# Kernel tuning notes

Measured on AMD Instinct MI355X. Metric: run time of the kernel, lower is better.

## Reference

```python
import jax, jax.numpy as jnp
import numpy as np

H = 1024   # hidden_dim
NH = 16    # num_heads
HD = H // NH  # head_dim = 64
B, S = 2, 2048
LN_EPS = 1e-5


def setup_inputs() -> dict:
    key = jax.random.key(0)
    ks = jax.random.split(key, 5)
    scale = 1.0 / np.sqrt(H)  # xavier-ish scale for stability
    return {
        "x": jax.random.normal(ks[0], (B, S, H), dtype=jnp.float32),
        "Wq": jax.random.normal(ks[1], (H, H), dtype=jnp.float32) * scale,
        "bq": jnp.zeros((H,), jnp.float32),
        "Wk": jax.random.normal(ks[2], (H, H), dtype=jnp.float32) * scale,
        "bk": jnp.zeros((H,), jnp.float32),
        "Wv": jax.random.normal(ks[3], (H, H), dtype=jnp.float32) * scale,
        "bv": jnp.zeros((H,), jnp.float32),
        "Wo": jax.random.normal(ks[4], (H, H), dtype=jnp.float32) * scale,
        "bo": jnp.zeros((H,), jnp.float32),
        "ln_gamma": jnp.ones((H,), jnp.float32),
        "ln_beta": jnp.zeros((H,), jnp.float32),
    }


def reference(x, Wq, bq, Wk, bk, Wv, bv, Wo, bo, ln_gamma, ln_beta):
    b, s, _ = x.shape
    # QKV projections, split heads: (b, nh, s, hd)
    def split_heads(t):
        return t.reshape(b, s, NH, HD).transpose(0, 2, 1, 3)
    Q = split_heads(x @ Wq + bq)
    K = split_heads(x @ Wk + bk)
    V = split_heads(x @ Wv + bv)
    # scaled dot-product with clamp (mask=None path)
    scores = jnp.einsum('bhqd,bhkd->bhqk', Q, K) / np.sqrt(HD).astype(np.float32)
    scores = jnp.clip(scores, -10000.0, 10000.0)
    attn = jax.nn.softmax(scores, axis=-1)
    # dropout is identity in eval mode
    ctx = jnp.einsum('bhqk,bhkd->bhqd', attn, V)
    ctx = ctx.transpose(0, 2, 1, 3).reshape(b, s, H)
    out = ctx @ Wo + bo
    # residual + LayerNorm
    y = out + x
    mu = jnp.mean(y, axis=-1, keepdims=True)
    var = jnp.mean(jnp.square(y - mu), axis=-1, keepdims=True)
    y = (y - mu) * jax.lax.rsqrt(var + LN_EPS)
    return y * ln_gamma + ln_beta
```

## Files before the change

kernel.cpp:

```cpp
#include <hip/hip_runtime.h>

typedef unsigned short u16;
typedef __attribute__((ext_vector_type(8))) short shortx8;
typedef __attribute__((ext_vector_type(4))) float floatx4;
typedef __attribute__((ext_vector_type(2))) unsigned uintx2;

#define GLD16(gp, lp) __builtin_amdgcn_global_load_lds( \
    (__attribute__((address_space(1))) void*)(gp), \
    (__attribute__((address_space(3))) void*)(lp), 16, 0, 0)

__device__ __forceinline__ u16 f2bf(float f) {
  union { float f; unsigned u; } v; v.f = f;
  unsigned r = v.u + 0x7FFFu + ((v.u >> 16) & 1u);
  return (u16)(r >> 16);
}

__device__ __forceinline__ unsigned bcast_u(float f) {
  union { float f; unsigned u; } v; v.f = f;
  return v.u;
}

__global__ __launch_bounds__(256) void cast_x_kernel(const float* __restrict__ x,
                                                     u16* __restrict__ xb, int n4) {
  int i = blockIdx.x * 256 + threadIdx.x;
  if (i < n4) {
    float4 v = ((const float4*)x)[i];
    ushort4 o;
    o.x = f2bf(v.x); o.y = f2bf(v.y); o.z = f2bf(v.z); o.w = f2bf(v.w);
    ((ushort4*)xb)[i] = o;
  }
}

__global__ __launch_bounds__(256) void transpose_cast_w(const float* __restrict__ Wq,
                                                        const float* __restrict__ Wk,
                                                        const float* __restrict__ Wv,
                                                        const float* __restrict__ Wo,
                                                        u16* __restrict__ Wt) {
  __shared__ u16 tile[32][33];
  int mat = blockIdx.z;
  const float* W = (mat == 0) ? Wq : (mat == 1) ? Wk : (mat == 2) ? Wv : Wo;
  u16* dst = Wt + (size_t)mat * 1024 * 1024;
  int n0 = blockIdx.x * 32, k0 = blockIdx.y * 32;
  int tx = threadIdx.x, ty = threadIdx.y;
  for (int i = 0; i < 4; ++i)
    tile[ty + i * 8][tx] = f2bf(W[(size_t)(k0 + ty + i * 8) * 1024 + n0 + tx]);
  __syncthreads();
  for (int i = 0; i < 4; ++i)
    dst[(size_t)(n0 + ty + i * 8) * 1024 + k0 + tx] = tile[tx][ty + i * 8];
}

__device__ __forceinline__ void gemm_tile_core(const u16* __restrict__ A,
                                               const u16* __restrict__ Bt,
                                               int m0, int n0,
                                               u16* As, u16* Bs,
                                               floatx4 (&acc)[4][4]) {
  const int tid = threadIdx.x;
  const int wave = tid >> 6, lane = tid & 63;
  const int lrow = lane >> 4, lcol = lane & 15;
  const int wm = wave >> 1, wn = wave & 1;

  for (int mi = 0; mi < 4; ++mi)
    for (int ni = 0; ni < 4; ++ni)
      acc[mi][ni] = (floatx4){0.f, 0.f, 0.f, 0.f};

  const u16* ap[4];
  const u16* bp[4];
  for (int l = 0; l < 4; ++l) {
    int g = (l * 4 + wave) * 64 + lane;
    int r = g >> 3, c = g & 7;
    int cc = (c ^ (r & 7)) * 8;
    ap[l] = A + (size_t)(m0 + r) * 1024 + cc;
    bp[l] = Bt + (size_t)(n0 + r) * 1024 + cc;
  }

  for (int k0 = 0; k0 < 1024; k0 += 64) {
    __syncthreads();
    for (int l = 0; l < 4; ++l) {
      GLD16(ap[l], As + (l * 4 + wave) * 512);
      GLD16(bp[l], Bs + (l * 4 + wave) * 512);
      ap[l] += 64; bp[l] += 64;
    }
    __syncthreads();
    for (int kk = 0; kk < 2; ++kk) {
      shortx8 af[4], bf[4];
      for (int mi = 0; mi < 4; ++mi) {
        int row = wm * 64 + mi * 16 + lcol;
        int gr = (kk * 4 + lrow) ^ (row & 7);
        af[mi] = *(const shortx8*)&As[row * 64 + gr * 8];
      }
      for (int ni = 0; ni < 4; ++ni) {
        int row = wn * 64 + ni * 16 + lcol;
        int gr = (kk * 4 + lrow) ^ (row & 7);
        bf[ni] = *(const shortx8*)&Bs[row * 64 + gr * 8];
      }
      for (int mi = 0; mi < 4; ++mi)
        for (int ni = 0; ni < 4; ++ni)
          acc[mi][ni] = __builtin_amdgcn_mfma_f32_16x16x32_bf16(af[mi], bf[ni], acc[mi][ni], 0, 0, 0);
    }
  }
}

__global__ __launch_bounds__(256) void qkv_gemm(const u16* __restrict__ xb,
                                                const u16* __restrict__ Wt,
                                                const float* __restrict__ bq,
                                                const float* __restrict__ bk,
                                                const float* __restrict__ bv,
                                                u16* __restrict__ Qh,
                                                u16* __restrict__ Kh,
                                                u16* __restrict__ Vth) {
  __shared__ u16 As[128 * 64];
  __shared__ u16 Bs[128 * 64];
  int m0 = blockIdx.x * 128;
  int mat = blockIdx.y >> 3;
  int n0 = (blockIdx.y & 7) * 128;
  floatx4 acc[4][4];
  gemm_tile_core(xb, Wt + (size_t)mat * 1024 * 1024, m0, n0, As, Bs, acc);

  const float* bias = (mat == 0) ? bq : (mat == 1) ? bk : bv;
  const int tid = threadIdx.x;
  const int wave = tid >> 6, lane = tid & 63;
  const int lrow = lane >> 4, lcol = lane & 15;
  const int wm = wave >> 1, wn = wave & 1;
  const float qscale = 0.18033688011f;

  for (int mi = 0; mi < 4; ++mi) {
    int mbase = m0 + wm * 64 + mi * 16 + lrow * 4;
    for (int ni = 0; ni < 4; ++ni) {
      int n = n0 + wn * 64 + ni * 16 + lcol;
      float bval = bias[n];
      int h = n >> 6, d = n & 63;
      if (mat < 2) {
        u16* dst = (mat == 0) ? Qh : Kh;
        float sc = (mat == 0) ? qscale : 1.0f;
        for (int r = 0; r < 4; ++r) {
          int m = mbase + r;
          int bb = m >> 11, s = m & 2047;
          dst[((size_t)(bb * 16 + h) * 2048 + s) * 64 + d] = f2bf((acc[mi][ni][r] + bval) * sc);
        }
      } else {
        int bb = mbase >> 11, s = mbase & 2047;
        ushort4 pk;
        pk.x = f2bf(acc[mi][ni][0] + bval);
        pk.y = f2bf(acc[mi][ni][1] + bval);
        pk.z = f2bf(acc[mi][ni][2] + bval);
        pk.w = f2bf(acc[mi][ni][3] + bval);
        *(ushort4*)&Vth[((size_t)(bb * 16 + h) * 64 + d) * 2048 + s] = pk;
      }
    }
  }
}

__global__ __launch_bounds__(256) void out_gemm(const u16* __restrict__ ctx,
                                                const u16* __restrict__ Wot,
                                                const float* __restrict__ bo,
                                                float* __restrict__ aout) {
  __shared__ u16 As[128 * 64];
  __shared__ u16 Bs[64 * 64];
  int m0 = blockIdx.x * 128;
  int n0 = blockIdx.y * 64;
  const int tid = threadIdx.x;
  const int wave = tid >> 6, lane = tid & 63;
  const int lrow = lane >> 4, lcol = lane & 15;
  const int wm = wave >> 1, wn = wave & 1;

  floatx4 acc[4][2];
  for (int mi = 0; mi < 4; ++mi)
    for (int ni = 0; ni < 2; ++ni)
      acc[mi][ni] = (floatx4){0.f, 0.f, 0.f, 0.f};

  const u16* ap[4];
  const u16* bp[2];
  for (int l = 0; l < 4; ++l) {
    int g = (l * 4 + wave) * 64 + lane;
    int r = g >> 3, c = g & 7;
    ap[l] = ctx + (size_t)(m0 + r) * 1024 + (c ^ (r & 7)) * 8;
  }
  for (int l = 0; l < 2; ++l) {
    int g = (l * 4 + wave) * 64 + lane;
    int r = g >> 3, c = g & 7;
    bp[l] = Wot + (size_t)(n0 + r) * 1024 + (c ^ (r & 7)) * 8;
  }

  for (int k0 = 0; k0 < 1024; k0 += 64) {
    __syncthreads();
    for (int l = 0; l < 4; ++l) { GLD16(ap[l], As + (l * 4 + wave) * 512); ap[l] += 64; }
    for (int l = 0; l < 2; ++l) { GLD16(bp[l], Bs + (l * 4 + wave) * 512); bp[l] += 64; }
    __syncthreads();
    for (int kk = 0; kk < 2; ++kk) {
      shortx8 af[4], bf[2];
      for (int mi = 0; mi < 4; ++mi) {
        int row = wm * 64 + mi * 16 + lcol;
        int gr = (kk * 4 + lrow) ^ (row & 7);
        af[mi] = *(const shortx8*)&As[row * 64 + gr * 8];
      }
      for (int ni = 0; ni < 2; ++ni) {
        int row = wn * 32 + ni * 16 + lcol;
        int gr = (kk * 4 + lrow) ^ (row & 7);
        bf[ni] = *(const shortx8*)&Bs[row * 64 + gr * 8];
      }
      for (int mi = 0; mi < 4; ++mi)
        for (int ni = 0; ni < 2; ++ni)
          acc[mi][ni] = __builtin_amdgcn_mfma_f32_16x16x32_bf16(af[mi], bf[ni], acc[mi][ni], 0, 0, 0);
    }
  }

  for (int mi = 0; mi < 4; ++mi) {
    int mbase = m0 + wm * 64 + mi * 16 + lrow * 4;
    for (int ni = 0; ni < 2; ++ni) {
      int n = n0 + wn * 32 + ni * 16 + lcol;
      float bval = bo[n];
      for (int r = 0; r < 4; ++r)
        aout[(size_t)(mbase + r) * 1024 + n] = acc[mi][ni][r] + bval;
    }
  }
}

__global__ __launch_bounds__(512) void attn_kernel(const u16* __restrict__ Qh,
                                                   const u16* __restrict__ Kh,
                                                   const u16* __restrict__ Vth,
                                                   u16* __restrict__ ctx) {
  __shared__ u16 QPs[128 * 64];
  __shared__ u16 Ks[2][64 * 64];
  __shared__ u16 Vs[2][64 * 64];

  int bh = blockIdx.x;
  int b = bh >> 4, h = bh & 15;
  int q0 = blockIdx.y * 128;
  int tid = threadIdx.x;
  int wave = tid >> 6, lane = tid & 63;
  int lrow = lane >> 4, lcol = lane & 15;

  const u16* Qg = Qh + ((size_t)bh * 2048 + q0) * 64;
  for (int l = 0; l < 2; ++l) {
    int g = (l * 8 + wave) * 64 + lane;
    int r = g >> 3, c = g & 7;
    GLD16(Qg + r * 64 + ((c ^ (r & 7)) * 8), QPs + (l * 8 + wave) * 512);
  }

  const u16* Kbase = Kh + (size_t)bh * 2048 * 64;
  const u16* Vbase = Vth + (size_t)bh * 64 * 2048;

  int g = wave * 64 + lane;
  int gr = g >> 3, gc = g & 7;
  int cc = (gc ^ (gr & 7)) * 8;
  const u16* kp = Kbase + (size_t)gr * 64 + cc;
  const u16* vp = Vbase + (size_t)gr * 2048 + cc;

  GLD16(kp, (u16*)Ks + wave * 512);
  GLD16(vp, (u16*)Vs + wave * 512);
  kp += 4096;
  vp += 64;
  __syncthreads();

  shortx8 qf[2];
  for (int kk = 0; kk < 2; ++kk) {
    int row = wave * 16 + lcol;
    int grr = (kk * 4 + lrow) ^ (row & 7);
    qf[kk] = *(const shortx8*)&QPs[row * 64 + grr * 8];
  }

  floatx4 o[4];
  float rs = 0.f;
  for (int dt = 0; dt < 4; ++dt) o[dt] = (floatx4){0.f, 0.f, 0.f, 0.f};

  for (int i = 0; i < 32; ++i) {
    int cur = i & 1;
    if (i < 31) {
      GLD16(kp, (u16*)Ks + (cur ^ 1) * 4096 + wave * 512);
      GLD16(vp, (u16*)Vs + (cur ^ 1) * 4096 + wave * 512);
      kp += 4096;
      vp += 64;
    }

    floatx4 sc[4];
    for (int kt = 0; kt < 4; ++kt)
      sc[kt] = (floatx4){0.f, 0.f, 0.f, 0.f};
    for (int kk = 0; kk < 2; ++kk) {
      for (int kt = 0; kt < 4; ++kt) {
        int row = kt * 16 + lcol;
        int grr = (kk * 4 + lrow) ^ (row & 7);
        shortx8 kf = *(const shortx8*)&Ks[cur][row * 64 + grr * 8];
        sc[kt] = __builtin_amdgcn_mfma_f32_16x16x32_bf16(kf, qf[kk], sc[kt], 0, 0, 0);
      }
    }

    for (int kt = 0; kt < 4; ++kt)
      for (int r = 0; r < 4; ++r) {
        float p = __builtin_amdgcn_exp2f(sc[kt][r]);
        sc[kt][r] = p;
        rs += p;
      }

    {
      int row = wave * 16 + lcol;
      for (int kt = 0; kt < 4; ++kt) {
        int gg = kt * 2 + (lrow >> 1);
        int addr = row * 64 + ((gg ^ (row & 7)) * 8) + (lrow & 1) * 4;
        unsigned t0 = bcast_u(sc[kt][0]) + 0x8000u;
        unsigned t1 = bcast_u(sc[kt][1]) + 0x8000u;
        unsigned t2 = bcast_u(sc[kt][2]) + 0x8000u;
        unsigned t3 = bcast_u(sc[kt][3]) + 0x8000u;
        uintx2 pk;
        pk.x = __builtin_amdgcn_perm(t1, t0, 0x07060302u);
        pk.y = __builtin_amdgcn_perm(t3, t2, 0x07060302u);
        *(uintx2*)&QPs[addr] = pk;
      }
    }

    for (int kk = 0; kk < 2; ++kk) {
      int prow = wave * 16 + lcol;
      int pgr = (kk * 4 + lrow) ^ (prow & 7);
      shortx8 pf = *(const shortx8*)&QPs[prow * 64 + pgr * 8];
      for (int dt = 0; dt < 4; ++dt) {
        int row = dt * 16 + lcol;
        int grr = (kk * 4 + lrow) ^ (row & 7);
        shortx8 vf = *(const shortx8*)&Vs[cur][row * 64 + grr * 8];
        o[dt] = __builtin_amdgcn_mfma_f32_16x16x32_bf16(vf, pf, o[dt], 0, 0, 0);
      }
    }
    __syncthreads();
  }

  {
    float l = rs;
    l += __shfl_xor(l, 16, 64);
    l += __shfl_xor(l, 32, 64);
    float inv = 1.0f / l;
    int s = q0 + wave * 16 + lcol;
    u16* dst = ctx + (size_t)(b * 2048 + s) * 1024 + h * 64 + lrow * 4;
    for (int dt = 0; dt < 4; ++dt) {
      ushort4 pk;
      pk.x = f2bf(o[dt][0] * inv);
      pk.y = f2bf(o[dt][1] * inv);
      pk.z = f2bf(o[dt][2] * inv);
      pk.w = f2bf(o[dt][3] * inv);
      *(ushort4*)(dst + dt * 16) = pk;
    }
  }
}

__global__ __launch_bounds__(256) void ln_kernel(const float* __restrict__ aout,
                                                 const float* __restrict__ x,
                                                 const float* __restrict__ gamma,
                                                 const float* __restrict__ beta,
                                                 float* __restrict__ out) {
  int row = blockIdx.x;
  int t = threadIdx.x;
  const float4* a4 = (const float4*)(aout + (size_t)row * 1024);
  const float4* x4 = (const float4*)(x + (size_t)row * 1024);
  float4 v = a4[t];
  float4 xv = x4[t];
  v.x += xv.x; v.y += xv.y; v.z += xv.z; v.w += xv.w;
  float s = v.x + v.y + v.z + v.w;
  float s2 = v.x * v.x + v.y * v.y + v.z * v.z + v.w * v.w;
  for (int off = 1; off < 64; off <<= 1) {
    s += __shfl_xor(s, off, 64);
    s2 += __shfl_xor(s2, off, 64);
  }
  __shared__ float red[8];
  int wave = t >> 6, lane = t & 63;
  if (lane == 0) { red[wave] = s; red[4 + wave] = s2; }
  __syncthreads();
  s = red[0] + red[1] + red[2] + red[3];
  s2 = red[4] + red[5] + red[6] + red[7];
  float mu = s * (1.0f / 1024.0f);
  float var = s2 * (1.0f / 1024.0f) - mu * mu;
  float rstd = rsqrtf(var + 1e-5f);
  float4 g = ((const float4*)gamma)[t];
  float4 be = ((const float4*)beta)[t];
  float4 y;
  y.x = (v.x - mu) * rstd * g.x + be.x;
  y.y = (v.y - mu) * rstd * g.y + be.y;
  y.z = (v.z - mu) * rstd * g.z + be.z;
  y.w = (v.w - mu) * rstd * g.w + be.w;
  ((float4*)(out + (size_t)row * 1024))[t] = y;
}

extern "C" void kernel_launch(void* const* d_in, const int* in_sizes, int n_in,
                              void* d_out, int out_size, void* d_ws, size_t ws_size,
                              hipStream_t stream) {
  const float* x     = (const float*)d_in[0];
  const float* Wq    = (const float*)d_in[1];
  const float* bq    = (const float*)d_in[2];
  const float* Wk    = (const float*)d_in[3];
  const float* bk    = (const float*)d_in[4];
  const float* Wv    = (const float*)d_in[5];
  const float* bv    = (const float*)d_in[6];
  const float* Wo    = (const float*)d_in[7];
  const float* bo    = (const float*)d_in[8];
  const float* gamma = (const float*)d_in[9];
  const float* beta  = (const float*)d_in[10];
  float* out = (float*)d_out;

  char* ws = (char*)d_ws;
  u16* xb   = (u16*)(ws);
  u16* Wt   = (u16*)(ws + ((size_t)8 << 20));
  u16* Qh   = (u16*)(ws + ((size_t)16 << 20));
  u16* Kh   = (u16*)(ws + ((size_t)24 << 20));
  u16* Vth  = (u16*)(ws + ((size_t)32 << 20));
  u16* ctx  = (u16*)(ws + ((size_t)40 << 20));
  float* aout = (float*)(ws + ((size_t)48 << 20));

  cast_x_kernel<<<4096, 256, 0, stream>>>(x, xb, 1048576);
  transpose_cast_w<<<dim3(32, 32, 4), dim3(32, 8), 0, stream>>>(Wq, Wk, Wv, Wo, Wt);
  qkv_gemm<<<dim3(32, 24), 256, 0, stream>>>(xb, Wt, bq, bk, bv, Qh, Kh, Vth);
  attn_kernel<<<dim3(32, 16), 512, 0, stream>>>(Qh, Kh, Vth, ctx);
  out_gemm<<<dim3(32, 16), 256, 0, stream>>>(ctx, Wt + (size_t)3 * 1024 * 1024, bo, aout);
  ln_kernel<<<4096, 256, 0, stream>>>(aout, x, gamma, beta, out);
}
```

Before: 207.7 us.

## Merge prep kernels, stage Q/K epilogue through LDS, MFMA row sums

Merges the x cast and weight transpose-cast into one launch. Routes the Q/K GEMM epilogue through a swizzled LDS tile so each thread writes 16-byte coalesced rows instead of scattered 2-byte stores. In attention, the softmax row sum is now taken with an extra MFMA against a ones vector, which replaces the scalar accumulation and shuffles. It also uses a packed bf16 convert where the builtin exists. The row sum now comes from bf16-rounded P, which slightly changes numerics and adds one MFMA per k-step.

```diff
diff --git a/kernel.cpp b/kernel.cpp
--- a/kernel.cpp
+++ b/kernel.cpp
@@ -15,38 +15,47 @@
   return (u16)(r >> 16);
 }
 
-__device__ __forceinline__ unsigned bcast_u(float f) {
-  union { float f; unsigned u; } v; v.f = f;
-  return v.u;
-}
-
-__global__ __launch_bounds__(256) void cast_x_kernel(const float* __restrict__ x,
-                                                     u16* __restrict__ xb, int n4) {
-  int i = blockIdx.x * 256 + threadIdx.x;
-  if (i < n4) {
+__device__ __forceinline__ unsigned pkbf(float a, float b) {
+#if __has_builtin(__builtin_amdgcn_cvt_pk_bf16_f32)
+  auto r = __builtin_amdgcn_cvt_pk_bf16_f32(a, b);
+  return __builtin_bit_cast(unsigned, r);
+#else
+  union { float f; unsigned u; } x, y; x.f = a; y.f = b;
+  return __builtin_amdgcn_perm(y.u + 0x8000u, x.u + 0x8000u, 0x07060302u);
+#endif
+}
+
+__global__ __launch_bounds__(256) void prep_kernel(const float* __restrict__ x,
+                                                   u16* __restrict__ xb,
+                                                   const float* __restrict__ Wq,
+                                                   const float* __restrict__ Wk,
+                                                   const float* __restrict__ Wv,
+                                                   const float* __restrict__ Wo,
+                                                   u16* __restrict__ Wt) {
+  __shared__ u16 tile[32][33];
+  int bid = blockIdx.x;
+  int tid = threadIdx.x;
+  if (bid < 4096) {
+    int i = bid * 256 + tid;
     float4 v = ((const float4*)x)[i];
-    ushort4 o;
-    o.x = f2bf(v.x); o.y = f2bf(v.y); o.z = f2bf(v.z); o.w = f2bf(v.w);
-    ((ushort4*)xb)[i] = o;
-  }
-}
-
-__global__ __launch_bounds__(256) void transpose_cast_w(const float* __restrict__ Wq,
-                                                        const float* __restrict__ Wk,
-                                                        const float* __restrict__ Wv,
-                                                        const float* __restrict__ Wo,
-                                                        u16* __restrict__ Wt) {
-  __shared__ u16 tile[32][33];
-  int mat = blockIdx.z;
-  const float* W = (mat == 0) ? Wq : (mat == 1) ? Wk : (mat == 2) ? Wv : Wo;
-  u16* dst = Wt + (size_t)mat * 1024 * 1024;
-  int n0 = blockIdx.x * 32, k0 = blockIdx.y * 32;
-  int tx = threadIdx.x, ty = threadIdx.y;
-  for (int i = 0; i < 4; ++i)
-    tile[ty + i * 8][tx] = f2bf(W[(size_t)(k0 + ty + i * 8) * 1024 + n0 + tx]);
-  __syncthreads();
-  for (int i = 0; i < 4; ++i)
-    dst[(size_t)(n0 + ty + i * 8) * 1024 + k0 + tx] = tile[tx][ty + i * 8];
+    uintx2 o;
+    o.x = pkbf(v.x, v.y);
+    o.y = pkbf(v.z, v.w);
+    ((uintx2*)xb)[i] = o;
+  } else {
+    int block = bid - 4096;
+    int mat = block >> 10;
+    int rem = block & 1023;
+    const float* W = (mat == 0) ? Wq : (mat == 1) ? Wk : (mat == 2) ? Wv : Wo;
+    u16* dst = Wt + (size_t)mat * 1024 * 1024;
+    int n0 = (rem & 31) * 32, k0 = (rem >> 5) * 32;
+    int tx = tid & 31, ty = tid >> 5;
+    for (int i = 0; i < 4; ++i)
+      tile[ty + i * 8][tx] = f2bf(W[(size_t)(k0 + ty + i * 8) * 1024 + n0 + tx]);
+    __syncthreads();
+    for (int i = 0; i < 4; ++i)
+      dst[(size_t)(n0 + ty + i * 8) * 1024 + k0 + tx] = tile[tx][ty + i * 8];
+  }
 }
 
 __device__ __forceinline__ void gemm_tile_core(const u16* __restrict__ A,
@@ -108,8 +117,9 @@
                                                 u16* __restrict__ Qh,
                                                 u16* __restrict__ Kh,
                                                 u16* __restrict__ Vth) {
-  __shared__ u16 As[128 * 64];
-  __shared__ u16 Bs[128 * 64];
+  __shared__ u16 sbuf[128 * 128];
+  u16* As = sbuf;
+  u16* Bs = sbuf + 128 * 64;
   int m0 = blockIdx.x * 128;
   int mat = blockIdx.y >> 3;
   int n0 = (blockIdx.y & 7) * 128;
@@ -123,28 +133,46 @@
   const int wm = wave >> 1, wn = wave & 1;
   const float qscale = 0.18033688011f;
 
-  for (int mi = 0; mi < 4; ++mi) {
-    int mbase = m0 + wm * 64 + mi * 16 + lrow * 4;
-    for (int ni = 0; ni < 4; ++ni) {
-      int n = n0 + wn * 64 + ni * 16 + lcol;
-      float bval = bias[n];
-      int h = n >> 6, d = n & 63;
-      if (mat < 2) {
-        u16* dst = (mat == 0) ? Qh : Kh;
-        float sc = (mat == 0) ? qscale : 1.0f;
+  if (mat < 2) {
+    u16* dst = (mat == 0) ? Qh : Kh;
+    float sc = (mat == 0) ? qscale : 1.0f;
+    __syncthreads();
+    for (int mi = 0; mi < 4; ++mi) {
+      int mb = wm * 64 + mi * 16 + lrow * 4;
+      for (int ni = 0; ni < 4; ++ni) {
+        int n = wn * 64 + ni * 16 + lcol;
+        float bval = bias[n0 + n];
         for (int r = 0; r < 4; ++r) {
-          int m = mbase + r;
-          int bb = m >> 11, s = m & 2047;
-          dst[((size_t)(bb * 16 + h) * 2048 + s) * 64 + d] = f2bf((acc[mi][ni][r] + bval) * sc);
+          int m = mb + r;
+          sbuf[m * 128 + (((n >> 3) ^ (m & 15)) * 8) + (n & 7)] =
+              f2bf((acc[mi][ni][r] + bval) * sc);
         }
-      } else {
-        int bb = mbase >> 11, s = mbase & 2047;
-        ushort4 pk;
-        pk.x = f2bf(acc[mi][ni][0] + bval);
-        pk.y = f2bf(acc[mi][ni][1] + bval);
-        pk.z = f2bf(acc[mi][ni][2] + bval);
-        pk.w = f2bf(acc[mi][ni][3] + bval);
-        *(ushort4*)&Vth[((size_t)(bb * 16 + h) * 64 + d) * 2048 + s] = pk;
+      }
+    }
+    __syncthreads();
+    int row = tid >> 1, half = tid & 1;
+    int m = m0 + row;
+    int bb = m >> 11, s = m & 2047;
+    for (int i = 0; i < 8; ++i) {
+      int cg = half * 8 + i;
+      int pg = cg ^ (row & 15);
+      shortx8 v = *(const shortx8*)&sbuf[row * 128 + pg * 8];
+      int ng = n0 + cg * 8;
+      int h = ng >> 6, d = ng & 63;
+      *(shortx8*)&dst[((size_t)(bb * 16 + h) * 2048 + s) * 64 + d] = v;
+    }
+  } else {
+    for (int mi = 0; mi < 4; ++mi) {
+      int mbase = m0 + wm * 64 + mi * 16 + lrow * 4;
+      int bb = mbase >> 11, s = mbase & 2047;
+      for (int ni = 0; ni < 4; ++ni) {
+        int n = n0 + wn * 64 + ni * 16 + lcol;
+        float bval = bias[n];
+        int h = n >> 6, d = n & 63;
+        uintx2 pk;
+        pk.x = pkbf(acc[mi][ni][0] + bval, acc[mi][ni][1] + bval);
+        pk.y = pkbf(acc[mi][ni][2] + bval, acc[mi][ni][3] + bval);
+        *(uintx2*)&Vth[((size_t)(bb * 16 + h) * 64 + d) * 2048 + s] = pk;
       }
     }
   }
@@ -259,8 +287,11 @@
     qf[kk] = *(const shortx8*)&QPs[row * 64 + grr * 8];
   }
 
+  const short one_bf = (short)0x3F80;
+  const shortx8 ones8 = {one_bf, one_bf, one_bf, one_bf, one_bf, one_bf, one_bf, one_bf};
+
   floatx4 o[4];
-  float rs = 0.f;
+  floatx4 lacc = (floatx4){0.f, 0.f, 0.f, 0.f};
   for (int dt = 0; dt < 4; ++dt) o[dt] = (floatx4){0.f, 0.f, 0.f, 0.f};
 
   for (int i = 0; i < 32; ++i) {
@@ -284,25 +315,18 @@
       }
     }
 
-    for (int kt = 0; kt < 4; ++kt)
-      for (int r = 0; r < 4; ++r) {
-        float p = __builtin_amdgcn_exp2f(sc[kt][r]);
-        sc[kt][r] = p;
-        rs += p;
-      }
-
     {
       int row = wave * 16 + lcol;
       for (int kt = 0; kt < 4; ++kt) {
+        float p0 = __builtin_amdgcn_exp2f(sc[kt][0]);
+        float p1 = __builtin_amdgcn_exp2f(sc[kt][1]);
+        float p2 = __builtin_amdgcn_exp2f(sc[kt][2]);
+        float p3 = __builtin_amdgcn_exp2f(sc[kt][3]);
         int gg = kt * 2 + (lrow >> 1);
         int addr = row * 64 + ((gg ^ (row & 7)) * 8) + (lrow & 1) * 4;
-        unsigned t0 = bcast_u(sc[kt][0]) + 0x8000u;
-        unsigned t1 = bcast_u(sc[kt][1]) + 0x8000u;
-        unsigned t2 = bcast_u(sc[kt][2]) + 0x8000u;
-        unsigned t3 = bcast_u(sc[kt][3]) + 0x8000u;
         uintx2 pk;
-        pk.x = __builtin_amdgcn_perm(t1, t0, 0x07060302u);
-        pk.y = __builtin_amdgcn_perm(t3, t2, 0x07060302u);
+        pk.x = pkbf(p0, p1);
+        pk.y = pkbf(p2, p3);
         *(uintx2*)&QPs[addr] = pk;
       }
     }
@@ -311,6 +335,7 @@
       int prow = wave * 16 + lcol;
       int pgr = (kk * 4 + lrow) ^ (prow & 7);
       shortx8 pf = *(const shortx8*)&QPs[prow * 64 + pgr * 8];
+      lacc = __builtin_amdgcn_mfma_f32_16x16x32_bf16(ones8, pf, lacc, 0, 0, 0);
       for (int dt = 0; dt < 4; ++dt) {
         int row = dt * 16 + lcol;
         int grr = (kk * 4 + lrow) ^ (row & 7);
@@ -322,19 +347,14 @@
   }
 
   {
-    float l = rs;
-    l += __shfl_xor(l, 16, 64);
-    l += __shfl_xor(l, 32, 64);
-    float inv = 1.0f / l;
+    float inv = 1.0f / lacc[0];
     int s = q0 + wave * 16 + lcol;
     u16* dst = ctx + (size_t)(b * 2048 + s) * 1024 + h * 64 + lrow * 4;
     for (int dt = 0; dt < 4; ++dt) {
-      ushort4 pk;
-      pk.x = f2bf(o[dt][0] * inv);
-      pk.y = f2bf(o[dt][1] * inv);
-      pk.z = f2bf(o[dt][2] * inv);
-      pk.w = f2bf(o[dt][3] * inv);
-      *(ushort4*)(dst + dt * 16) = pk;
+      uintx2 pk;
+      pk.x = pkbf(o[dt][0] * inv, o[dt][1] * inv);
+      pk.y = pkbf(o[dt][2] * inv, o[dt][3] * inv);
+      *(uintx2*)(dst + dt * 16) = pk;
     }
   }
 }
@@ -401,8 +421,7 @@
   u16* ctx  = (u16*)(ws + ((size_t)40 << 20));
   float* aout = (float*)(ws + ((size_t)48 << 20));
 
-  cast_x_kernel<<<4096, 256, 0, stream>>>(x, xb, 1048576);
-  transpose_cast_w<<<dim3(32, 32, 4), dim3(32, 8), 0, stream>>>(Wq, Wk, Wv, Wo, Wt);
+  prep_kernel<<<8192, 256, 0, stream>>>(x, xb, Wq, Wk, Wv, Wo, Wt);
   qkv_gemm<<<dim3(32, 24), 256, 0, stream>>>(xb, Wt, bq, bk, bv, Qh, Kh, Vth);
   attn_kernel<<<dim3(32, 16), 512, 0, stream>>>(Qh, Kh, Vth, ctx);
   out_gemm<<<dim3(32, 16), 256, 0, stream>>>(ctx, Wt + (size_t)3 * 1024 * 1024, bo, aout);
```

Result: no change. 205.5 us (-1.1%).
